# Kernel optimization log

Hardware: AMD Instinct MI355X
Metric: run time of the kernel (lower is better)

The kernel has to match this reference:

```python
import jax, jax.numpy as jnp
import numpy as np

HIDDEN = 2048
INTER = 1408
NUM_EXPERTS = 8
TOP_K = 2


def setup_inputs() -> dict:
    key = jax.random.key(0)
    k_x, k_rw, k_gu, k_dn = jax.random.split(key, 4)
    x = jax.random.normal(k_x, (2, 2048, HIDDEN), dtype=jnp.float32)
    router_weight = jax.random.normal(k_rw, (NUM_EXPERTS, HIDDEN), dtype=jnp.float32)
    gate_up_proj = jax.random.normal(k_gu, (NUM_EXPERTS, 2 * INTER, HIDDEN), dtype=jnp.float32) * 0.02
    down_proj = jax.random.normal(k_dn, (NUM_EXPERTS, HIDDEN, INTER), dtype=jnp.float32) * 0.02
    return {"x": x, "router_weight": router_weight, "gate_up_proj": gate_up_proj, "down_proj": down_proj}


def reference(x, router_weight, gate_up_proj, down_proj):
    E = router_weight.shape[0]
    xf = x.reshape(-1, x.shape[-1])  # [T, D]
    # Router: logits -> float32 softmax -> top-k -> renormalize
    logits = jnp.einsum('td,ed->te', xf, router_weight)
    scores = jax.nn.softmax(logits.astype(jnp.float32), axis=-1)
    topv, topi = jax.lax.top_k(scores, TOP_K)          # [T, K]
    topv = topv / jnp.sum(topv, axis=-1, keepdims=True)
    topv = topv.astype(logits.dtype)
    # Combine weights per (token, expert): zero for unselected experts,
    # so dense per-expert compute below reproduces the sparse dispatch math.
    comb = jnp.einsum('tk,tke->te', topv, jax.nn.one_hot(topi, E, dtype=topv.dtype))  # [T, E]
    # Per-expert SwiGLU FFN, dense over experts
    gu = jnp.einsum('td,efd->etf', xf, gate_up_proj)    # [E, T, 2*inter]
    gate, up = jnp.split(gu, 2, axis=-1)
    h = jax.nn.silu(gate) * up                          # [E, T, inter]
    eo = jnp.einsum('eti,edi->etd', h, down_proj)       # [E, T, D]
    out = jnp.einsum('etd,te->td', eo, comb)            # [T, D]
    return out
```

## Files before the change

kernel.cpp:

```cpp
#include <hip/hip_runtime.h>
#include <hip/hip_bf16.h>
#include <stdint.h>

#define HIDDEN 2048
#define INTER  1408
#define NE     8
#define NTOK   4096
#define MAXTILES 72

typedef __attribute__((ext_vector_type(8))) short short8;
typedef __attribute__((ext_vector_type(16))) float f32x16;

typedef const __attribute__((address_space(1))) unsigned char* gp1_t;
typedef __attribute__((address_space(3))) unsigned char* lp3_t;

__device__ __forceinline__ void lds_cp16(const void* g, void* l) {
    __builtin_amdgcn_global_load_lds((gp1_t)g, (lp3_t)l, 16, 0, 0);
}

__device__ __forceinline__ short8 ldswz(const __hip_bfloat16 (*S)[64], int r, int col) {
    return *(const short8*)&S[r][(((col >> 3) ^ (r & 7)) << 3)];
}

__device__ __forceinline__ float bf2f(short s) {
    union { float f; unsigned u; } u; u.u = ((unsigned)(unsigned short)s) << 16; return u.f;
}

#define C1 (NE * 2 * INTER * HIDDEN / 4)
#define C2 (NE * HIDDEN * INTER / 4)
__global__ void cvt_w_kernel(const float* __restrict__ gu, const float* __restrict__ dn,
                             __hip_bfloat16* __restrict__ gub, __hip_bfloat16* __restrict__ dnb) {
    long c = (long)blockIdx.x * blockDim.x + threadIdx.x;
    const float* s; __hip_bfloat16* d; long o;
    if (c < C1) { s = gu; d = gub; o = c; }
    else        { s = dn; d = dnb; o = c - C1; }
    o *= 4;
    float4 v = *(const float4*)(s + o);
    *(__hip_bfloat162*)(d + o)     = __float22bfloat162_rn(make_float2(v.x, v.y));
    *(__hip_bfloat162*)(d + o + 2) = __float22bfloat162_rn(make_float2(v.z, v.w));
}

__global__ void router_kernel(const float* __restrict__ x, const float* __restrict__ rw,
                              int* __restrict__ counts, int* __restrict__ topk_e,
                              float* __restrict__ topk_w, __hip_bfloat16* __restrict__ xb) {
    int wave = threadIdx.x >> 6;
    int lane = threadIdx.x & 63;
    int t = blockIdx.x * 4 + wave;
    const float4* xr = (const float4*)(x + (size_t)t * HIDDEN);
    __hip_bfloat16* xbr = xb + (size_t)t * HIDDEN;
    float acc[NE] = {0.f,0.f,0.f,0.f,0.f,0.f,0.f,0.f};
    #pragma unroll
    for (int c = lane; c < HIDDEN / 4; c += 64) {
        float4 v = xr[c];
        *(__hip_bfloat162*)(xbr + c * 4)     = __float22bfloat162_rn(make_float2(v.x, v.y));
        *(__hip_bfloat162*)(xbr + c * 4 + 2) = __float22bfloat162_rn(make_float2(v.z, v.w));
        #pragma unroll
        for (int e = 0; e < NE; ++e) {
            float4 w = ((const float4*)(rw + e * HIDDEN))[c];
            acc[e] += v.x * w.x + v.y * w.y + v.z * w.z + v.w * w.w;
        }
    }
    #pragma unroll
    for (int e = 0; e < NE; ++e) {
        #pragma unroll
        for (int off = 32; off > 0; off >>= 1) acc[e] += __shfl_xor(acc[e], off, 64);
    }
    if (lane == 0) {
        int i1 = 0; float v1 = acc[0];
        for (int e = 1; e < NE; ++e) if (acc[e] > v1) { v1 = acc[e]; i1 = e; }
        int i2 = -1; float v2 = -3.0e38f;
        for (int e = 0; e < NE; ++e) if (e != i1 && acc[e] > v2) { v2 = acc[e]; i2 = e; }
        float w1 = 1.f / (1.f + expf(v2 - v1));
        float w2 = 1.f - w1;
        topk_e[t * 2 + 0] = i1; topk_e[t * 2 + 1] = i2;
        topk_w[t * 2 + 0] = w1; topk_w[t * 2 + 1] = w2;
        atomicAdd(&counts[i1], 1);
        atomicAdd(&counts[i2], 1);
    }
}

__global__ void scan_kernel(const int* __restrict__ counts, int* __restrict__ offsets,
                            int* __restrict__ cursor, int* __restrict__ tiles,
                            int* __restrict__ n_tiles) {
    if (threadIdx.x == 0) {
        int s = 0, nt = 0;
        for (int e = 0; e < NE; ++e) {
            offsets[e] = s; cursor[e] = s;
            int c = counts[e]; s += c;
            for (int mt = 0; mt * 128 < c; ++mt) tiles[nt++] = (e << 16) | mt;
        }
        n_tiles[0] = nt;
    }
}

__global__ void scatter_kernel(const int* __restrict__ topk_e, const float* __restrict__ topk_w,
                               int* __restrict__ cursor, int* __restrict__ slot_tid,
                               float* __restrict__ slot_w, int* __restrict__ tok2slot) {
    int k = blockIdx.x * blockDim.x + threadIdx.x;
    if (k >= NTOK * 2) return;
    int e = topk_e[k];
    int slot = atomicAdd(&cursor[e], 1);
    slot_tid[slot] = k >> 1;
    slot_w[slot]   = topk_w[k];
    tok2slot[k]    = slot;
}

__global__ __launch_bounds__(256) void gemm1_kernel(
    const __hip_bfloat16* __restrict__ xb,
    const __hip_bfloat16* __restrict__ gub,
    const int* __restrict__ counts, const int* __restrict__ offsets,
    const int* __restrict__ tiles, const int* __restrict__ n_tiles,
    const int* __restrict__ slot_tid, const float* __restrict__ slot_w,
    __hip_bfloat16* __restrict__ h)
{
    const int ti = blockIdx.y;
    if (ti >= n_tiles[0]) return;
    const int tile = tiles[ti];
    const int e  = tile >> 16;
    const int mt = tile & 0xffff;
    const int nt = blockIdx.x;
    const int count = counts[e];
    const int off = offsets[e];

    __shared__ __hip_bfloat16 As[128][64];
    __shared__ __hip_bfloat16 Bs[128][64];

    const int tid  = threadIdx.x;
    const int wave = tid >> 6;
    const int lane = tid & 63;
    const int wm = wave >> 1, wn = wave & 1;
    const int l31 = lane & 31;
    const int fk  = (lane >> 5) * 8;

    const __hip_bfloat16* asrc[4];
    const __hip_bfloat16* bsrc[4];
    #pragma unroll
    for (int j = 0; j < 4; ++j) {
        int fs  = j * 256 + tid;
        int row = fs >> 3;
        int c8  = (fs & 7) ^ (row & 7);
        int rg  = mt * 128 + row;
        int rc  = rg < count ? rg : count - 1;
        int tok = slot_tid[off + rc];
        asrc[j] = xb + (size_t)tok * HIDDEN + c8 * 8;
        int within = row & 63, sel = within >> 5, idx = within & 31;
        int hc  = nt * 64 + (row >> 6) * 32 + idx;
        int grow = sel ? (INTER + hc) : hc;
        bsrc[j] = gub + ((size_t)e * 2 * INTER + grow) * HIDDEN + c8 * 8;
    }

    f32x16 accg[2], accu[2];
    #pragma unroll
    for (int mi = 0; mi < 2; ++mi) { accg[mi] = (f32x16)0.f; accu[mi] = (f32x16)0.f; }

    for (int k0 = 0; k0 < HIDDEN; k0 += 64) {
        #pragma unroll
        for (int j = 0; j < 4; ++j) {
            lds_cp16(asrc[j] + k0, (__hip_bfloat16*)As + (j * 256 + tid) * 8);
            lds_cp16(bsrc[j] + k0, (__hip_bfloat16*)Bs + (j * 256 + tid) * 8);
        }
        __syncthreads();
        #pragma unroll
        for (int kk = 0; kk < 64; kk += 16) {
            short8 a0 = ldswz(As, wm * 64 +      l31, kk + fk);
            short8 a1 = ldswz(As, wm * 64 + 32 + l31, kk + fk);
            short8 bg = ldswz(Bs, wn * 64 +      l31, kk + fk);
            short8 bu = ldswz(Bs, wn * 64 + 32 + l31, kk + fk);
            accg[0] = __builtin_amdgcn_mfma_f32_32x32x16_bf16(a0, bg, accg[0], 0, 0, 0);
            accg[1] = __builtin_amdgcn_mfma_f32_32x32x16_bf16(a1, bg, accg[1], 0, 0, 0);
            accu[0] = __builtin_amdgcn_mfma_f32_32x32x16_bf16(a0, bu, accu[0], 0, 0, 0);
            accu[1] = __builtin_amdgcn_mfma_f32_32x32x16_bf16(a1, bu, accu[1], 0, 0, 0);
        }
        __syncthreads();
    }

    #pragma unroll
    for (int mi = 0; mi < 2; ++mi) {
        #pragma unroll
        for (int reg = 0; reg < 16; ++reg) {
            int row = wm * 64 + mi * 32 + (reg & 3) + 8 * (reg >> 2) + 4 * (lane >> 5);
            int rg  = mt * 128 + row;
            if (rg < count) {
                float wgt = slot_w[off + rg];
                float g = accg[mi][reg];
                float u = accu[mi][reg];
                float hv = g / (1.f + __expf(-g)) * u * wgt;
                h[(size_t)(off + rg) * INTER + nt * 64 + wn * 32 + l31] = __float2bfloat16(hv);
            }
        }
    }
}

__global__ __launch_bounds__(256) void gemm2_kernel(
    const __hip_bfloat16* __restrict__ h,
    const __hip_bfloat16* __restrict__ dnb,
    const int* __restrict__ counts, const int* __restrict__ offsets,
    const int* __restrict__ tiles, const int* __restrict__ n_tiles,
    __hip_bfloat16* __restrict__ eo)
{
    const int ti = blockIdx.y;
    if (ti >= n_tiles[0]) return;
    const int tile = tiles[ti];
    const int e  = tile >> 16;
    const int mt = tile & 0xffff;
    const int nt = blockIdx.x;
    const int count = counts[e];
    const int off = offsets[e];

    __shared__ __hip_bfloat16 As[128][64];
    __shared__ __hip_bfloat16 Bs[128][64];

    const int tid  = threadIdx.x;
    const int wave = tid >> 6;
    const int lane = tid & 63;
    const int wm = wave >> 1, wn = wave & 1;
    const int l31 = lane & 31;
    const int fk  = (lane >> 5) * 8;

    const __hip_bfloat16* asrc[4];
    const __hip_bfloat16* bsrc[4];
    #pragma unroll
    for (int j = 0; j < 4; ++j) {
        int fs  = j * 256 + tid;
        int row = fs >> 3;
        int c8  = (fs & 7) ^ (row & 7);
        asrc[j] = h + (size_t)(off + mt * 128 + row) * INTER + c8 * 8;
        bsrc[j] = dnb + ((size_t)e * HIDDEN + nt * 128 + row) * INTER + c8 * 8;
    }

    f32x16 acc[2][2];
    #pragma unroll
    for (int mi = 0; mi < 2; ++mi)
        #pragma unroll
        for (int nj = 0; nj < 2; ++nj) acc[mi][nj] = (f32x16)0.f;

    for (int k0 = 0; k0 < INTER; k0 += 64) {
        #pragma unroll
        for (int j = 0; j < 4; ++j) {
            lds_cp16(asrc[j] + k0, (__hip_bfloat16*)As + (j * 256 + tid) * 8);
            lds_cp16(bsrc[j] + k0, (__hip_bfloat16*)Bs + (j * 256 + tid) * 8);
        }
        __syncthreads();
        #pragma unroll
        for (int kk = 0; kk < 64; kk += 16) {
            short8 a0 = ldswz(As, wm * 64 +      l31, kk + fk);
            short8 a1 = ldswz(As, wm * 64 + 32 + l31, kk + fk);
            short8 b0 = ldswz(Bs, wn * 64 +      l31, kk + fk);
            short8 b1 = ldswz(Bs, wn * 64 + 32 + l31, kk + fk);
            acc[0][0] = __builtin_amdgcn_mfma_f32_32x32x16_bf16(a0, b0, acc[0][0], 0, 0, 0);
            acc[0][1] = __builtin_amdgcn_mfma_f32_32x32x16_bf16(a0, b1, acc[0][1], 0, 0, 0);
            acc[1][0] = __builtin_amdgcn_mfma_f32_32x32x16_bf16(a1, b0, acc[1][0], 0, 0, 0);
            acc[1][1] = __builtin_amdgcn_mfma_f32_32x32x16_bf16(a1, b1, acc[1][1], 0, 0, 0);
        }
        __syncthreads();
    }

    #pragma unroll
    for (int mi = 0; mi < 2; ++mi) {
        #pragma unroll
        for (int reg = 0; reg < 16; ++reg) {
            int row = wm * 64 + mi * 32 + (reg & 3) + 8 * (reg >> 2) + 4 * (lane >> 5);
            int rg  = mt * 128 + row;
            if (rg < count) {
                size_t base = (size_t)(off + rg) * HIDDEN + nt * 128 + wn * 64;
                eo[base +      l31] = __float2bfloat16(acc[mi][0][reg]);
                eo[base + 32 + l31] = __float2bfloat16(acc[mi][1][reg]);
            }
        }
    }
}

__global__ void combine_kernel(const __hip_bfloat16* __restrict__ eo,
                               const int* __restrict__ tok2slot,
                               float* __restrict__ out) {
    int idx = blockIdx.x * blockDim.x + threadIdx.x;
    int t = idx >> 8;
    int c = (idx & 255) * 8;
    int s1 = tok2slot[t * 2], s2 = tok2slot[t * 2 + 1];
    short8 v1 = *(const short8*)(eo + (size_t)s1 * HIDDEN + c);
    short8 v2 = *(const short8*)(eo + (size_t)s2 * HIDDEN + c);
    float4 o0, o1;
    o0.x = bf2f(v1[0]) + bf2f(v2[0]); o0.y = bf2f(v1[1]) + bf2f(v2[1]);
    o0.z = bf2f(v1[2]) + bf2f(v2[2]); o0.w = bf2f(v1[3]) + bf2f(v2[3]);
    o1.x = bf2f(v1[4]) + bf2f(v2[4]); o1.y = bf2f(v1[5]) + bf2f(v2[5]);
    o1.z = bf2f(v1[6]) + bf2f(v2[6]); o1.w = bf2f(v1[7]) + bf2f(v2[7]);
    float* op = out + (size_t)t * HIDDEN + c;
    *(float4*)op = o0;
    *(float4*)(op + 4) = o1;
}

extern "C" void kernel_launch(void* const* d_in, const int* in_sizes, int n_in,
                              void* d_out, int out_size, void* d_ws, size_t ws_size,
                              hipStream_t stream)
{
    (void)in_sizes; (void)n_in; (void)ws_size; (void)out_size;
    const float* x  = (const float*)d_in[0];
    const float* rw = (const float*)d_in[1];
    const float* gu = (const float*)d_in[2];
    const float* dn = (const float*)d_in[3];

    char* p = (char*)d_ws;
    auto take = [&](size_t bytes) { char* r = p; p += (bytes + 255) & ~(size_t)255; return r; };
    __hip_bfloat16* xb  = (__hip_bfloat16*)take((size_t)NTOK * HIDDEN * 2);
    __hip_bfloat16* gub = (__hip_bfloat16*)take((size_t)NE * 2 * INTER * HIDDEN * 2);
    __hip_bfloat16* dnb = (__hip_bfloat16*)take((size_t)NE * HIDDEN * INTER * 2);
    __hip_bfloat16* hbuf= (__hip_bfloat16*)take((size_t)(2 * NTOK + 128) * INTER * 2);
    int*   counts   = (int*)take(64);
    int*   offsets  = (int*)take(64);
    int*   cursor   = (int*)take(64);
    int*   ntile    = (int*)take(64);
    int*   tiles    = (int*)take(MAXTILES * 4);
    int*   topk_e   = (int*)take((size_t)NTOK * 2 * 4);
    float* topk_w   = (float*)take((size_t)NTOK * 2 * 4);
    int*   slot_tid = (int*)take((size_t)(2 * NTOK + 128) * 4);
    float* slot_w   = (float*)take((size_t)(2 * NTOK + 128) * 4);
    int*   tok2slot = (int*)take((size_t)NTOK * 2 * 4);
    __hip_bfloat16* eo = gub;

    hipMemsetAsync(counts, 0, 64, stream);

    cvt_w_kernel<<<dim3((C1 + C2) / 256), 256, 0, stream>>>(gu, dn, gub, dnb);

    router_kernel<<<dim3(NTOK / 4), 256, 0, stream>>>(x, rw, counts, topk_e, topk_w, xb);
    scan_kernel<<<dim3(1), 64, 0, stream>>>(counts, offsets, cursor, tiles, ntile);
    scatter_kernel<<<dim3((NTOK * 2) / 256), 256, 0, stream>>>(topk_e, topk_w, cursor,
                                                               slot_tid, slot_w, tok2slot);

    gemm1_kernel<<<dim3(INTER / 64, MAXTILES), 256, 0, stream>>>(
        xb, gub, counts, offsets, tiles, ntile, slot_tid, slot_w, hbuf);
    gemm2_kernel<<<dim3(HIDDEN / 128, MAXTILES), 256, 0, stream>>>(
        hbuf, dnb, counts, offsets, tiles, ntile, eo);
    combine_kernel<<<dim3(NTOK * HIDDEN / 8 / 256), 256, 0, stream>>>(
        eo, tok2slot, (float*)d_out);
}
```

Before: 692.0 us.

## Enlarge MoE GEMM tiles with 512-thread blocks and double-buffered LDS pipeline

Both grouped GEMMs now run 512-thread blocks with larger tiles: 256x128 for gate/up and 128x256 for down. Each uses two dynamic-LDS buffers, so the next K-slice is fetched with global_load_lds while MFMAs run on the current one, and waits go through explicit vmcnt and raw barriers. The MFMA shape changes from 32x32x16 to 16x16x32, with setprio raised around the MFMA bursts, and a separate tile list is built for the larger gemm1 row tile. The aim is more reuse per loaded byte and hiding global latency behind compute. The cost is much larger LDS use, which limits occupancy, and more padding waste on partial expert tiles.

```diff
diff --git a/kernel.cpp b/kernel.cpp
--- a/kernel.cpp
+++ b/kernel.cpp
@@ -6,10 +6,11 @@
 #define INTER  1408
 #define NE     8
 #define NTOK   4096
-#define MAXTILES 72
+#define MAXT1  40
+#define MAXT2  72
 
 typedef __attribute__((ext_vector_type(8))) short short8;
-typedef __attribute__((ext_vector_type(16))) float f32x16;
+typedef __attribute__((ext_vector_type(4))) float f32x4;
 
 typedef const __attribute__((address_space(1))) unsigned char* gp1_t;
 typedef __attribute__((address_space(3))) unsigned char* lp3_t;
@@ -18,8 +19,8 @@
     __builtin_amdgcn_global_load_lds((gp1_t)g, (lp3_t)l, 16, 0, 0);
 }
 
-__device__ __forceinline__ short8 ldswz(const __hip_bfloat16 (*S)[64], int r, int col) {
-    return *(const short8*)&S[r][(((col >> 3) ^ (r & 7)) << 3)];
+__device__ __forceinline__ short8 ldswz64(const __hip_bfloat16* S, int r, int ck) {
+    return *(const short8*)&S[r * 64 + ((ck ^ (r & 7)) << 3)];
 }
 
 __device__ __forceinline__ float bf2f(short s) {
@@ -80,16 +81,18 @@
 }
 
 __global__ void scan_kernel(const int* __restrict__ counts, int* __restrict__ offsets,
-                            int* __restrict__ cursor, int* __restrict__ tiles,
-                            int* __restrict__ n_tiles) {
+                            int* __restrict__ cursor, int* __restrict__ tiles1,
+                            int* __restrict__ tiles2, int* __restrict__ n_tiles) {
     if (threadIdx.x == 0) {
-        int s = 0, nt = 0;
+        int s = 0, nt1 = 0, nt2 = 0;
         for (int e = 0; e < NE; ++e) {
             offsets[e] = s; cursor[e] = s;
             int c = counts[e]; s += c;
-            for (int mt = 0; mt * 128 < c; ++mt) tiles[nt++] = (e << 16) | mt;
-        }
-        n_tiles[0] = nt;
+            for (int mt = 0; mt * 256 < c; ++mt) tiles1[nt1++] = (e << 16) | mt;
+            for (int mt = 0; mt * 128 < c; ++mt) tiles2[nt2++] = (e << 16) | mt;
+        }
+        n_tiles[0] = nt1;
+        n_tiles[1] = nt2;
     }
 }
 
@@ -105,7 +108,7 @@
     tok2slot[k]    = slot;
 }
 
-__global__ __launch_bounds__(256) void gemm1_kernel(
+__global__ __launch_bounds__(512, 2) void gemm1_kernel(
     const __hip_bfloat16* __restrict__ xb,
     const __hip_bfloat16* __restrict__ gub,
     const int* __restrict__ counts, const int* __restrict__ offsets,
@@ -122,76 +125,111 @@
     const int count = counts[e];
     const int off = offsets[e];
 
-    __shared__ __hip_bfloat16 As[128][64];
-    __shared__ __hip_bfloat16 Bs[128][64];
+    extern __shared__ __hip_bfloat16 smem[];
+    __hip_bfloat16* A0 = smem;
+    __hip_bfloat16* B0 = smem + 16384;
+    __hip_bfloat16* A1 = smem + 32768;
+    __hip_bfloat16* B1 = smem + 49152;
 
     const int tid  = threadIdx.x;
     const int wave = tid >> 6;
     const int lane = tid & 63;
-    const int wm = wave >> 1, wn = wave & 1;
-    const int l31 = lane & 31;
-    const int fk  = (lane >> 5) * 8;
+    const int wm = wave >> 2, wn = wave & 3;
+    const int l15 = lane & 15;
+    const int q   = lane >> 4;
 
     const __hip_bfloat16* asrc[4];
     const __hip_bfloat16* bsrc[4];
     #pragma unroll
     for (int j = 0; j < 4; ++j) {
-        int fs  = j * 256 + tid;
+        int fs  = j * 512 + tid;
         int row = fs >> 3;
         int c8  = (fs & 7) ^ (row & 7);
-        int rg  = mt * 128 + row;
+        int rg  = mt * 256 + row;
         int rc  = rg < count ? rg : count - 1;
         int tok = slot_tid[off + rc];
         asrc[j] = xb + (size_t)tok * HIDDEN + c8 * 8;
-        int within = row & 63, sel = within >> 5, idx = within & 31;
-        int hc  = nt * 64 + (row >> 6) * 32 + idx;
+        int p = row >> 5, sel = (row >> 4) & 1, idx = row & 15;
+        int hc = nt * 128 + p * 16 + idx;
         int grow = sel ? (INTER + hc) : hc;
-        bsrc[j] = gub + ((size_t)e * 2 * INTER + grow) * HIDDEN + c8 * 8;
-    }
-
-    f32x16 accg[2], accu[2];
-    #pragma unroll
-    for (int mi = 0; mi < 2; ++mi) { accg[mi] = (f32x16)0.f; accu[mi] = (f32x16)0.f; }
-
-    for (int k0 = 0; k0 < HIDDEN; k0 += 64) {
-        #pragma unroll
-        for (int j = 0; j < 4; ++j) {
-            lds_cp16(asrc[j] + k0, (__hip_bfloat16*)As + (j * 256 + tid) * 8);
-            lds_cp16(bsrc[j] + k0, (__hip_bfloat16*)Bs + (j * 256 + tid) * 8);
-        }
-        __syncthreads();
-        #pragma unroll
-        for (int kk = 0; kk < 64; kk += 16) {
-            short8 a0 = ldswz(As, wm * 64 +      l31, kk + fk);
-            short8 a1 = ldswz(As, wm * 64 + 32 + l31, kk + fk);
-            short8 bg = ldswz(Bs, wn * 64 +      l31, kk + fk);
-            short8 bu = ldswz(Bs, wn * 64 + 32 + l31, kk + fk);
-            accg[0] = __builtin_amdgcn_mfma_f32_32x32x16_bf16(a0, bg, accg[0], 0, 0, 0);
-            accg[1] = __builtin_amdgcn_mfma_f32_32x32x16_bf16(a1, bg, accg[1], 0, 0, 0);
-            accu[0] = __builtin_amdgcn_mfma_f32_32x32x16_bf16(a0, bu, accu[0], 0, 0, 0);
-            accu[1] = __builtin_amdgcn_mfma_f32_32x32x16_bf16(a1, bu, accu[1], 0, 0, 0);
-        }
-        __syncthreads();
-    }
-
-    #pragma unroll
-    for (int mi = 0; mi < 2; ++mi) {
-        #pragma unroll
-        for (int reg = 0; reg < 16; ++reg) {
-            int row = wm * 64 + mi * 32 + (reg & 3) + 8 * (reg >> 2) + 4 * (lane >> 5);
-            int rg  = mt * 128 + row;
+        bsrc[j] = gub + ((size_t)(e * 2 * INTER + grow)) * HIDDEN + c8 * 8;
+    }
+
+    f32x4 acc[8][4];
+    #pragma unroll
+    for (int mf = 0; mf < 8; ++mf)
+        #pragma unroll
+        for (int nf = 0; nf < 4; ++nf) acc[mf][nf] = (f32x4)0.f;
+
+    #pragma unroll
+    for (int j = 0; j < 4; ++j) lds_cp16(asrc[j], (__hip_bfloat16*)A0 + (j * 512 + tid) * 8);
+    #pragma unroll
+    for (int j = 0; j < 4; ++j) lds_cp16(bsrc[j], (__hip_bfloat16*)B0 + (j * 512 + tid) * 8);
+
+    #pragma unroll 2
+    for (int t = 0; t < 32; ++t) {
+        const __hip_bfloat16* Ac = (t & 1) ? A1 : A0;
+        const __hip_bfloat16* Bc = (t & 1) ? B1 : B0;
+        __hip_bfloat16* An = (t & 1) ? A0 : A1;
+        __hip_bfloat16* Bn = (t & 1) ? B0 : B1;
+        if (t + 1 < 32) {
+            const int k0 = (t + 1) * 64;
+            #pragma unroll
+            for (int j = 0; j < 4; ++j) lds_cp16(asrc[j] + k0, An + (j * 512 + tid) * 8);
+            #pragma unroll
+            for (int j = 0; j < 4; ++j) lds_cp16(bsrc[j] + k0, Bn + (j * 512 + tid) * 8);
+            asm volatile("s_waitcnt vmcnt(8)" ::: "memory");
+        } else {
+            asm volatile("s_waitcnt vmcnt(0)" ::: "memory");
+        }
+        __builtin_amdgcn_sched_barrier(0);
+        __builtin_amdgcn_s_barrier();
+        asm volatile("" ::: "memory");
+        __builtin_amdgcn_sched_barrier(0);
+        #pragma unroll
+        for (int kh = 0; kh < 2; ++kh) {
+            const int ck = kh * 4 + q;
+            short8 bfr[4], afr[8];
+            #pragma unroll
+            for (int nf = 0; nf < 4; ++nf) bfr[nf] = ldswz64(Bc, wn * 64 + nf * 16 + l15, ck);
+            #pragma unroll
+            for (int mf = 0; mf < 8; ++mf) afr[mf] = ldswz64(Ac, wm * 128 + mf * 16 + l15, ck);
+            __builtin_amdgcn_s_setprio(1);
+            #pragma unroll
+            for (int mf = 0; mf < 8; ++mf)
+                #pragma unroll
+                for (int nf = 0; nf < 4; ++nf)
+                    acc[mf][nf] = __builtin_amdgcn_mfma_f32_16x16x32_bf16(afr[mf], bfr[nf], acc[mf][nf], 0, 0, 0);
+            __builtin_amdgcn_s_setprio(0);
+        }
+        __builtin_amdgcn_sched_barrier(0);
+        __builtin_amdgcn_s_barrier();
+        asm volatile("" ::: "memory");
+        __builtin_amdgcn_sched_barrier(0);
+    }
+
+    #pragma unroll
+    for (int mf = 0; mf < 8; ++mf) {
+        #pragma unroll
+        for (int reg = 0; reg < 4; ++reg) {
+            int row = wm * 128 + mf * 16 + q * 4 + reg;
+            int rg  = mt * 256 + row;
             if (rg < count) {
                 float wgt = slot_w[off + rg];
-                float g = accg[mi][reg];
-                float u = accu[mi][reg];
-                float hv = g / (1.f + __expf(-g)) * u * wgt;
-                h[(size_t)(off + rg) * INTER + nt * 64 + wn * 32 + l31] = __float2bfloat16(hv);
+                #pragma unroll
+                for (int g = 0; g < 2; ++g) {
+                    float gv = acc[mf][2 * g + 0][reg];
+                    float uv = acc[mf][2 * g + 1][reg];
+                    float hv = gv / (1.f + __expf(-gv)) * uv * wgt;
+                    h[(size_t)(off + rg) * INTER + nt * 128 + (wn * 2 + g) * 16 + l15] =
+                        __float2bfloat16(hv);
+                }
             }
         }
     }
 }
 
-__global__ __launch_bounds__(256) void gemm2_kernel(
+__global__ __launch_bounds__(512, 2) void gemm2_kernel(
     const __hip_bfloat16* __restrict__ h,
     const __hip_bfloat16* __restrict__ dnb,
     const int* __restrict__ counts, const int* __restrict__ offsets,
@@ -199,7 +237,7 @@
     __hip_bfloat16* __restrict__ eo)
 {
     const int ti = blockIdx.y;
-    if (ti >= n_tiles[0]) return;
+    if (ti >= n_tiles[1]) return;
     const int tile = tiles[ti];
     const int e  = tile >> 16;
     const int mt = tile & 0xffff;
@@ -207,64 +245,100 @@
     const int count = counts[e];
     const int off = offsets[e];
 
-    __shared__ __hip_bfloat16 As[128][64];
-    __shared__ __hip_bfloat16 Bs[128][64];
+    extern __shared__ __hip_bfloat16 smem[];
+    __hip_bfloat16* A0 = smem;
+    __hip_bfloat16* B0 = smem + 8192;
+    __hip_bfloat16* A1 = smem + 24576;
+    __hip_bfloat16* B1 = smem + 32768;
 
     const int tid  = threadIdx.x;
     const int wave = tid >> 6;
     const int lane = tid & 63;
-    const int wm = wave >> 1, wn = wave & 1;
-    const int l31 = lane & 31;
-    const int fk  = (lane >> 5) * 8;
-
-    const __hip_bfloat16* asrc[4];
+    const int wm = wave >> 2, wn = wave & 3;
+    const int l15 = lane & 15;
+    const int q   = lane >> 4;
+
+    const __hip_bfloat16* asrc[2];
     const __hip_bfloat16* bsrc[4];
     #pragma unroll
-    for (int j = 0; j < 4; ++j) {
-        int fs  = j * 256 + tid;
+    for (int j = 0; j < 2; ++j) {
+        int fs  = j * 512 + tid;
         int row = fs >> 3;
         int c8  = (fs & 7) ^ (row & 7);
         asrc[j] = h + (size_t)(off + mt * 128 + row) * INTER + c8 * 8;
-        bsrc[j] = dnb + ((size_t)e * HIDDEN + nt * 128 + row) * INTER + c8 * 8;
-    }
-
-    f32x16 acc[2][2];
-    #pragma unroll
-    for (int mi = 0; mi < 2; ++mi)
-        #pragma unroll
-        for (int nj = 0; nj < 2; ++nj) acc[mi][nj] = (f32x16)0.f;
-
-    for (int k0 = 0; k0 < INTER; k0 += 64) {
-        #pragma unroll
-        for (int j = 0; j < 4; ++j) {
-            lds_cp16(asrc[j] + k0, (__hip_bfloat16*)As + (j * 256 + tid) * 8);
-            lds_cp16(bsrc[j] + k0, (__hip_bfloat16*)Bs + (j * 256 + tid) * 8);
-        }
-        __syncthreads();
-        #pragma unroll
-        for (int kk = 0; kk < 64; kk += 16) {
-            short8 a0 = ldswz(As, wm * 64 +      l31, kk + fk);
-            short8 a1 = ldswz(As, wm * 64 + 32 + l31, kk + fk);
-            short8 b0 = ldswz(Bs, wn * 64 +      l31, kk + fk);
-            short8 b1 = ldswz(Bs, wn * 64 + 32 + l31, kk + fk);
-            acc[0][0] = __builtin_amdgcn_mfma_f32_32x32x16_bf16(a0, b0, acc[0][0], 0, 0, 0);
-            acc[0][1] = __builtin_amdgcn_mfma_f32_32x32x16_bf16(a0, b1, acc[0][1], 0, 0, 0);
-            acc[1][0] = __builtin_amdgcn_mfma_f32_32x32x16_bf16(a1, b0, acc[1][0], 0, 0, 0);
-            acc[1][1] = __builtin_amdgcn_mfma_f32_32x32x16_bf16(a1, b1, acc[1][1], 0, 0, 0);
-        }
-        __syncthreads();
-    }
-
-    #pragma unroll
-    for (int mi = 0; mi < 2; ++mi) {
-        #pragma unroll
-        for (int reg = 0; reg < 16; ++reg) {
-            int row = wm * 64 + mi * 32 + (reg & 3) + 8 * (reg >> 2) + 4 * (lane >> 5);
+    }
+    #pragma unroll
+    for (int j = 0; j < 4; ++j) {
+        int fs  = j * 512 + tid;
+        int row = fs >> 3;
+        int c8  = (fs & 7) ^ (row & 7);
+        bsrc[j] = dnb + ((size_t)(e * HIDDEN + nt * 256 + row)) * INTER + c8 * 8;
+    }
+
+    f32x4 acc[4][4];
+    #pragma unroll
+    for (int mf = 0; mf < 4; ++mf)
+        #pragma unroll
+        for (int nf = 0; nf < 4; ++nf) acc[mf][nf] = (f32x4)0.f;
+
+    #pragma unroll
+    for (int j = 0; j < 2; ++j) lds_cp16(asrc[j], (__hip_bfloat16*)A0 + (j * 512 + tid) * 8);
+    #pragma unroll
+    for (int j = 0; j < 4; ++j) lds_cp16(bsrc[j], (__hip_bfloat16*)B0 + (j * 512 + tid) * 8);
+
+    #pragma unroll 2
+    for (int t = 0; t < 22; ++t) {
+        const __hip_bfloat16* Ac = (t & 1) ? A1 : A0;
+        const __hip_bfloat16* Bc = (t & 1) ? B1 : B0;
+        __hip_bfloat16* An = (t & 1) ? A0 : A1;
+        __hip_bfloat16* Bn = (t & 1) ? B0 : B1;
+        if (t + 1 < 22) {
+            const int k0 = (t + 1) * 64;
+            #pragma unroll
+            for (int j = 0; j < 2; ++j) lds_cp16(asrc[j] + k0, An + (j * 512 + tid) * 8);
+            #pragma unroll
+            for (int j = 0; j < 4; ++j) lds_cp16(bsrc[j] + k0, Bn + (j * 512 + tid) * 8);
+            asm volatile("s_waitcnt vmcnt(6)" ::: "memory");
+        } else {
+            asm volatile("s_waitcnt vmcnt(0)" ::: "memory");
+        }
+        __builtin_amdgcn_sched_barrier(0);
+        __builtin_amdgcn_s_barrier();
+        asm volatile("" ::: "memory");
+        __builtin_amdgcn_sched_barrier(0);
+        #pragma unroll
+        for (int kh = 0; kh < 2; ++kh) {
+            const int ck = kh * 4 + q;
+            short8 bfr[4], afr[4];
+            #pragma unroll
+            for (int nf = 0; nf < 4; ++nf) bfr[nf] = ldswz64(Bc, wn * 64 + nf * 16 + l15, ck);
+            #pragma unroll
+            for (int mf = 0; mf < 4; ++mf) afr[mf] = ldswz64(Ac, wm * 64 + mf * 16 + l15, ck);
+            __builtin_amdgcn_s_setprio(1);
+            #pragma unroll
+            for (int mf = 0; mf < 4; ++mf)
+                #pragma unroll
+                for (int nf = 0; nf < 4; ++nf)
+                    acc[mf][nf] = __builtin_amdgcn_mfma_f32_16x16x32_bf16(afr[mf], bfr[nf], acc[mf][nf], 0, 0, 0);
+            __builtin_amdgcn_s_setprio(0);
+        }
+        __builtin_amdgcn_sched_barrier(0);
+        __builtin_amdgcn_s_barrier();
+        asm volatile("" ::: "memory");
+        __builtin_amdgcn_sched_barrier(0);
+    }
+
+    #pragma unroll
+    for (int mf = 0; mf < 4; ++mf) {
+        #pragma unroll
+        for (int reg = 0; reg < 4; ++reg) {
+            int row = wm * 64 + mf * 16 + q * 4 + reg;
             int rg  = mt * 128 + row;
             if (rg < count) {
-                size_t base = (size_t)(off + rg) * HIDDEN + nt * 128 + wn * 64;
-                eo[base +      l31] = __float2bfloat16(acc[mi][0][reg]);
-                eo[base + 32 + l31] = __float2bfloat16(acc[mi][1][reg]);
+                size_t base = (size_t)(off + rg) * HIDDEN + nt * 256 + wn * 64;
+                #pragma unroll
+                for (int nf = 0; nf < 4; ++nf)
+                    eo[base + nf * 16 + l15] = __float2bfloat16(acc[mf][nf][reg]);
             }
         }
     }
@@ -304,32 +378,38 @@
     __hip_bfloat16* xb  = (__hip_bfloat16*)take((size_t)NTOK * HIDDEN * 2);
     __hip_bfloat16* gub = (__hip_bfloat16*)take((size_t)NE * 2 * INTER * HIDDEN * 2);
     __hip_bfloat16* dnb = (__hip_bfloat16*)take((size_t)NE * HIDDEN * INTER * 2);
-    __hip_bfloat16* hbuf= (__hip_bfloat16*)take((size_t)(2 * NTOK + 128) * INTER * 2);
+    __hip_bfloat16* hbuf= (__hip_bfloat16*)take((size_t)(2 * NTOK + 256) * INTER * 2);
     int*   counts   = (int*)take(64);
     int*   offsets  = (int*)take(64);
     int*   cursor   = (int*)take(64);
     int*   ntile    = (int*)take(64);
-    int*   tiles    = (int*)take(MAXTILES * 4);
+    int*   tiles1   = (int*)take(MAXT1 * 4);
+    int*   tiles2   = (int*)take(MAXT2 * 4);
     int*   topk_e   = (int*)take((size_t)NTOK * 2 * 4);
     float* topk_w   = (float*)take((size_t)NTOK * 2 * 4);
-    int*   slot_tid = (int*)take((size_t)(2 * NTOK + 128) * 4);
-    float* slot_w   = (float*)take((size_t)(2 * NTOK + 128) * 4);
+    int*   slot_tid = (int*)take((size_t)(2 * NTOK + 256) * 4);
+    float* slot_w   = (float*)take((size_t)(2 * NTOK + 256) * 4);
     int*   tok2slot = (int*)take((size_t)NTOK * 2 * 4);
     __hip_bfloat16* eo = gub;
 
+    hipFuncSetAttribute((const void*)gemm1_kernel,
+                        hipFuncAttributeMaxDynamicSharedMemorySize, 131072);
+    hipFuncSetAttribute((const void*)gemm2_kernel,
+                        hipFuncAttributeMaxDynamicSharedMemorySize, 98304);
+
     hipMemsetAsync(counts, 0, 64, stream);
 
     cvt_w_kernel<<<dim3((C1 + C2) / 256), 256, 0, stream>>>(gu, dn, gub, dnb);
 
     router_kernel<<<dim3(NTOK / 4), 256, 0, stream>>>(x, rw, counts, topk_e, topk_w, xb);
-    scan_kernel<<<dim3(1), 64, 0, stream>>>(counts, offsets, cursor, tiles, ntile);
+    scan_kernel<<<dim3(1), 64, 0, stream>>>(counts, offsets, cursor, tiles1, tiles2, ntile);
     scatter_kernel<<<dim3((NTOK * 2) / 256), 256, 0, stream>>>(topk_e, topk_w, cursor,
                                                                slot_tid, slot_w, tok2slot);
 
-    gemm1_kernel<<<dim3(INTER / 64, MAXTILES), 256, 0, stream>>>(
-        xb, gub, counts, offsets, tiles, ntile, slot_tid, slot_w, hbuf);
-    gemm2_kernel<<<dim3(HIDDEN / 128, MAXTILES), 256, 0, stream>>>(
-        hbuf, dnb, counts, offsets, tiles, ntile, eo);
+    gemm1_kernel<<<dim3(INTER / 128, MAXT1), 512, 131072, stream>>>(
+        xb, gub, counts, offsets, tiles1, ntile, slot_tid, slot_w, hbuf);
+    gemm2_kernel<<<dim3(HIDDEN / 256, MAXT2), 512, 98304, stream>>>(
+        hbuf, dnb, counts, offsets, tiles2, ntile, eo);
     combine_kernel<<<dim3(NTOK * HIDDEN / 8 / 256), 256, 0, stream>>>(
         eo, tok2slot, (float*)d_out);
 }
```

Measured after the change: 738.2 us. 6.7% more time.

## Rewrite grouped MoE GEMMs as 256x256 pipelined 8-wave kernel with double-buffered LDS

Applied to the files above, without the earlier changes.

Replaces the two 128x128 single-buffered grouped GEMM kernels with one templated 512-thread kernel that computes 256x256 tiles. It uses 16x16x32 MFMAs, a swizzled 128KB dynamic LDS layout, and an explicit software pipeline in which async global-to-LDS loads for later k-tiles overlap the MFMAs, with manual vmcnt waits and barriers. The intent is more data reuse per tile and hidden load latency. In exchange it uses larger tiles, so per-expert padding waste grows, the grid has fewer blocks, and register pressure is high.

```diff
diff --git a/kernel.cpp b/kernel.cpp
--- a/kernel.cpp
+++ b/kernel.cpp
@@ -6,20 +6,16 @@
 #define INTER  1408
 #define NE     8
 #define NTOK   4096
-#define MAXTILES 72
+#define MAXT   40
 
 typedef __attribute__((ext_vector_type(8))) short short8;
-typedef __attribute__((ext_vector_type(16))) float f32x16;
+typedef __attribute__((ext_vector_type(4))) float f32x4;
 
 typedef const __attribute__((address_space(1))) unsigned char* gp1_t;
 typedef __attribute__((address_space(3))) unsigned char* lp3_t;
 
 __device__ __forceinline__ void lds_cp16(const void* g, void* l) {
     __builtin_amdgcn_global_load_lds((gp1_t)g, (lp3_t)l, 16, 0, 0);
-}
-
-__device__ __forceinline__ short8 ldswz(const __hip_bfloat16 (*S)[64], int r, int col) {
-    return *(const short8*)&S[r][(((col >> 3) ^ (r & 7)) << 3)];
 }
 
 __device__ __forceinline__ float bf2f(short s) {
@@ -87,7 +83,7 @@
         for (int e = 0; e < NE; ++e) {
             offsets[e] = s; cursor[e] = s;
             int c = counts[e]; s += c;
-            for (int mt = 0; mt * 128 < c; ++mt) tiles[nt++] = (e << 16) | mt;
+            for (int mt = 0; mt * 256 < c; ++mt) tiles[nt++] = (e << 16) | mt;
         }
         n_tiles[0] = nt;
     }
@@ -105,14 +101,71 @@
     tok2slot[k]    = slot;
 }
 
-__global__ __launch_bounds__(256) void gemm1_kernel(
-    const __hip_bfloat16* __restrict__ xb,
-    const __hip_bfloat16* __restrict__ gub,
+
+#define FENCE asm volatile("" ::: "memory")
+#define W_V8  asm volatile("s_waitcnt vmcnt(8)" ::: "memory")
+#define W_V4  asm volatile("s_waitcnt vmcnt(4)" ::: "memory")
+#define W_V0  asm volatile("s_waitcnt vmcnt(0)" ::: "memory")
+#define W_NONE do {} while (0)
+#define BAR do { __builtin_amdgcn_sched_barrier(0); FENCE; \
+                 __builtin_amdgcn_s_barrier(); FENCE; } while (0)
+#define LGKM0 do { asm volatile("s_waitcnt lgkmcnt(0)" ::: "memory"); \
+                   __builtin_amdgcn_sched_barrier(0); } while (0)
+
+#define DSA(Rg, mf) (*(const short8*)((Rg) + laneA + (mf) * 512))
+#define DSB(Rg, nf) (*(const short8*)((Rg) + laneB + (nf) * 512))
+
+#define MFMA16(NFP) do { \
+    __builtin_amdgcn_s_setprio(1); \
+    _Pragma("unroll") \
+    for (int mf_ = 0; mf_ < 8; ++mf_) { \
+        acc[mf_][(NFP)*2+0] = __builtin_amdgcn_mfma_f32_16x16x32_bf16(afr[mf_], bfr[0], acc[mf_][(NFP)*2+0], 0, 0, 0); \
+        acc[mf_][(NFP)*2+1] = __builtin_amdgcn_mfma_f32_16x16x32_bf16(afr[mf_], bfr[1], acc[mf_][(NFP)*2+1], 0, 0, 0); \
+    } \
+    __builtin_amdgcn_s_setprio(0); \
+    __builtin_amdgcn_sched_barrier(0); \
+} while (0)
+
+#define KTILE(T, S01, S23, W1, W3) do { \
+    const int b_ = (T) & 1; \
+    const __hip_bfloat16* RA0_ = smem + (((b_ << 2) | 0) << 13); \
+    const __hip_bfloat16* RA1_ = smem + (((b_ << 2) | 1) << 13); \
+    const __hip_bfloat16* RB0_ = smem + (((b_ << 2) | 2) << 13); \
+    const __hip_bfloat16* RB1_ = smem + (((b_ << 2) | 3) << 13); \
+     \
+    _Pragma("unroll") for (int mf_ = 0; mf_ < 8; ++mf_) afr[mf_] = DSA(RA0_, mf_); \
+    bfr[0] = DSB(RB0_, 0); bfr[1] = DSB(RB0_, 1); \
+    if (S01) stage(0, 1, (T) + 1, b_ ^ 1); \
+    LGKM0; MFMA16(0); BAR; \
+     \
+    bfr[0] = DSB(RB0_, 2); bfr[1] = DSB(RB0_, 3); \
+    if (S01) stage(1, 1, (T) + 1, b_ ^ 1); \
+    LGKM0; MFMA16(1); \
+    W1; BAR; \
+     \
+    _Pragma("unroll") for (int mf_ = 0; mf_ < 8; ++mf_) afr[mf_] = DSA(RA1_, mf_); \
+    bfr[0] = DSB(RB1_, 0); bfr[1] = DSB(RB1_, 1); \
+    if (S23) stage(0, 0, (T) + 2, b_); \
+    LGKM0; MFMA16(0); BAR; \
+     \
+    bfr[0] = DSB(RB1_, 2); bfr[1] = DSB(RB1_, 3); \
+    if (S23) stage(1, 0, (T) + 2, b_); \
+    LGKM0; MFMA16(1); \
+    W3; BAR; \
+} while (0)
+
+template<int WHICH>
+__global__ __launch_bounds__(512, 2) void moe_gemm(
+    const __hip_bfloat16* __restrict__ Ag,
+    const __hip_bfloat16* __restrict__ Bg,
     const int* __restrict__ counts, const int* __restrict__ offsets,
     const int* __restrict__ tiles, const int* __restrict__ n_tiles,
     const int* __restrict__ slot_tid, const float* __restrict__ slot_w,
-    __hip_bfloat16* __restrict__ h)
+    __hip_bfloat16* __restrict__ Out)
 {
+    constexpr int KDIM = (WHICH == 1) ? HIDDEN : INTER;
+    constexpr int NT   = KDIM / 64;
+
     const int ti = blockIdx.y;
     if (ti >= n_tiles[0]) return;
     const int tile = tiles[ti];
@@ -122,149 +175,103 @@
     const int count = counts[e];
     const int off = offsets[e];
 
-    __shared__ __hip_bfloat16 As[128][64];
-    __shared__ __hip_bfloat16 Bs[128][64];
+    extern __shared__ __hip_bfloat16 smem[];
 
     const int tid  = threadIdx.x;
     const int wave = tid >> 6;
     const int lane = tid & 63;
-    const int wm = wave >> 1, wn = wave & 1;
-    const int l31 = lane & 31;
-    const int fk  = (lane >> 5) * 8;
-
-    const __hip_bfloat16* asrc[4];
-    const __hip_bfloat16* bsrc[4];
+    const int wm = wave >> 2, wn = wave & 3;
+    const int l15 = lane & 15;
+    const int q   = lane >> 4;
+    const int sw  = (l15 >> 1) & 3;
+
+    const int laneA = (wm * 128 + l15) * 32 + ((q ^ sw) << 3);
+    const int laneB = (wn * 64  + l15) * 32 + ((q ^ sw) << 3);
+
+    const __hip_bfloat16* PA[2];
+    const __hip_bfloat16* PB[2];
     #pragma unroll
-    for (int j = 0; j < 4; ++j) {
-        int fs  = j * 256 + tid;
-        int row = fs >> 3;
-        int c8  = (fs & 7) ^ (row & 7);
-        int rg  = mt * 128 + row;
+    for (int j = 0; j < 2; ++j) {
+        int cs  = j * 512 + tid;
+        int row = cs >> 2;
+        int kc  = (cs & 3) ^ ((row >> 1) & 3);
+        int rg  = mt * 256 + row;
         int rc  = rg < count ? rg : count - 1;
-        int tok = slot_tid[off + rc];
-        asrc[j] = xb + (size_t)tok * HIDDEN + c8 * 8;
-        int within = row & 63, sel = within >> 5, idx = within & 31;
-        int hc  = nt * 64 + (row >> 6) * 32 + idx;
-        int grow = sel ? (INTER + hc) : hc;
-        bsrc[j] = gub + ((size_t)e * 2 * INTER + grow) * HIDDEN + c8 * 8;
-    }
-
-    f32x16 accg[2], accu[2];
+        if constexpr (WHICH == 1) {
+            int tok = slot_tid[off + rc];
+            PA[j] = Ag + (size_t)tok * HIDDEN + kc * 8;
+            int p = row >> 5, sel = (row >> 4) & 1, idx = row & 15;
+            int hc = nt * 128 + p * 16 + idx;
+            int grow = sel ? (INTER + hc) : hc;
+            PB[j] = Bg + ((size_t)(e * 2 * INTER + grow)) * HIDDEN + kc * 8;
+        } else {
+            PA[j] = Ag + (size_t)(off + rc) * INTER + kc * 8;
+            PB[j] = Bg + ((size_t)(e * HIDDEN + nt * 256 + row)) * INTER + kc * 8;
+        }
+    }
+
+    auto stage = [&](int m, int kh, int kt, int b) {
+        __hip_bfloat16* L = smem + (size_t)(((b << 2) | (m << 1) | kh) << 13);
+        const __hip_bfloat16* s0 = (m ? PB[0] : PA[0]) + kt * 64 + kh * 32;
+        const __hip_bfloat16* s1 = (m ? PB[1] : PA[1]) + kt * 64 + kh * 32;
+        lds_cp16(s0, L + tid * 8);
+        lds_cp16(s1, L + (512 + tid) * 8);
+    };
+
+    f32x4 acc[8][4];
     #pragma unroll
-    for (int mi = 0; mi < 2; ++mi) { accg[mi] = (f32x16)0.f; accu[mi] = (f32x16)0.f; }
-
-    for (int k0 = 0; k0 < HIDDEN; k0 += 64) {
-        #pragma unroll
-        for (int j = 0; j < 4; ++j) {
-            lds_cp16(asrc[j] + k0, (__hip_bfloat16*)As + (j * 256 + tid) * 8);
-            lds_cp16(bsrc[j] + k0, (__hip_bfloat16*)Bs + (j * 256 + tid) * 8);
-        }
-        __syncthreads();
-        #pragma unroll
-        for (int kk = 0; kk < 64; kk += 16) {
-            short8 a0 = ldswz(As, wm * 64 +      l31, kk + fk);
-            short8 a1 = ldswz(As, wm * 64 + 32 + l31, kk + fk);
-            short8 bg = ldswz(Bs, wn * 64 +      l31, kk + fk);
-            short8 bu = ldswz(Bs, wn * 64 + 32 + l31, kk + fk);
-            accg[0] = __builtin_amdgcn_mfma_f32_32x32x16_bf16(a0, bg, accg[0], 0, 0, 0);
-            accg[1] = __builtin_amdgcn_mfma_f32_32x32x16_bf16(a1, bg, accg[1], 0, 0, 0);
-            accu[0] = __builtin_amdgcn_mfma_f32_32x32x16_bf16(a0, bu, accu[0], 0, 0, 0);
-            accu[1] = __builtin_amdgcn_mfma_f32_32x32x16_bf16(a1, bu, accu[1], 0, 0, 0);
-        }
-        __syncthreads();
-    }
-
-    #pragma unroll
-    for (int mi = 0; mi < 2; ++mi) {
-        #pragma unroll
-        for (int reg = 0; reg < 16; ++reg) {
-            int row = wm * 64 + mi * 32 + (reg & 3) + 8 * (reg >> 2) + 4 * (lane >> 5);
-            int rg  = mt * 128 + row;
-            if (rg < count) {
-                float wgt = slot_w[off + rg];
-                float g = accg[mi][reg];
-                float u = accu[mi][reg];
-                float hv = g / (1.f + __expf(-g)) * u * wgt;
-                h[(size_t)(off + rg) * INTER + nt * 64 + wn * 32 + l31] = __float2bfloat16(hv);
+    for (int mf = 0; mf < 8; ++mf)
+        #pragma unroll
+        for (int nf = 0; nf < 4; ++nf) acc[mf][nf] = (f32x4)0.f;
+
+    short8 afr[8], bfr[2];
+
+    stage(0, 0, 0, 0); stage(1, 0, 0, 0);
+    stage(0, 1, 0, 0); stage(1, 1, 0, 0);
+    stage(0, 0, 1, 1); stage(1, 0, 1, 1);
+    W_V8; BAR;
+
+    #pragma unroll 2
+    for (int t = 0; t < NT - 2; ++t) {
+        KTILE(t, 1, 1, W_V8, W_V8);
+    }
+    KTILE(NT - 2, 1, 0, W_V8, W_V4);
+    KTILE(NT - 1, 0, 0, W_V0, W_NONE);
+    W_V0;
+
+    if constexpr (WHICH == 1) {
+        #pragma unroll
+        for (int mf = 0; mf < 8; ++mf) {
+            #pragma unroll
+            for (int reg = 0; reg < 4; ++reg) {
+                int row = wm * 128 + mf * 16 + q * 4 + reg;
+                int rg  = mt * 256 + row;
+                if (rg < count) {
+                    float wgt = slot_w[off + rg];
+                    #pragma unroll
+                    for (int g = 0; g < 2; ++g) {
+                        float gv = acc[mf][2 * g + 0][reg];
+                        float uv = acc[mf][2 * g + 1][reg];
+                        float hv = gv / (1.f + __expf(-gv)) * uv * wgt;
+                        Out[(size_t)(off + rg) * INTER + nt * 128 + (wn * 2 + g) * 16 + l15] =
+                            __float2bfloat16(hv);
+                    }
+                }
             }
         }
-    }
-}
-
-__global__ __launch_bounds__(256) void gemm2_kernel(
-    const __hip_bfloat16* __restrict__ h,
-    const __hip_bfloat16* __restrict__ dnb,
-    const int* __restrict__ counts, const int* __restrict__ offsets,
-    const int* __restrict__ tiles, const int* __restrict__ n_tiles,
-    __hip_bfloat16* __restrict__ eo)
-{
-    const int ti = blockIdx.y;
-    if (ti >= n_tiles[0]) return;
-    const int tile = tiles[ti];
-    const int e  = tile >> 16;
-    const int mt = tile & 0xffff;
-    const int nt = blockIdx.x;
-    const int count = counts[e];
-    const int off = offsets[e];
-
-    __shared__ __hip_bfloat16 As[128][64];
-    __shared__ __hip_bfloat16 Bs[128][64];
-
-    const int tid  = threadIdx.x;
-    const int wave = tid >> 6;
-    const int lane = tid & 63;
-    const int wm = wave >> 1, wn = wave & 1;
-    const int l31 = lane & 31;
-    const int fk  = (lane >> 5) * 8;
-
-    const __hip_bfloat16* asrc[4];
-    const __hip_bfloat16* bsrc[4];
-    #pragma unroll
-    for (int j = 0; j < 4; ++j) {
-        int fs  = j * 256 + tid;
-        int row = fs >> 3;
-        int c8  = (fs & 7) ^ (row & 7);
-        asrc[j] = h + (size_t)(off + mt * 128 + row) * INTER + c8 * 8;
-        bsrc[j] = dnb + ((size_t)e * HIDDEN + nt * 128 + row) * INTER + c8 * 8;
-    }
-
-    f32x16 acc[2][2];
-    #pragma unroll
-    for (int mi = 0; mi < 2; ++mi)
-        #pragma unroll
-        for (int nj = 0; nj < 2; ++nj) acc[mi][nj] = (f32x16)0.f;
-
-    for (int k0 = 0; k0 < INTER; k0 += 64) {
-        #pragma unroll
-        for (int j = 0; j < 4; ++j) {
-            lds_cp16(asrc[j] + k0, (__hip_bfloat16*)As + (j * 256 + tid) * 8);
-            lds_cp16(bsrc[j] + k0, (__hip_bfloat16*)Bs + (j * 256 + tid) * 8);
-        }
-        __syncthreads();
-        #pragma unroll
-        for (int kk = 0; kk < 64; kk += 16) {
-            short8 a0 = ldswz(As, wm * 64 +      l31, kk + fk);
-            short8 a1 = ldswz(As, wm * 64 + 32 + l31, kk + fk);
-            short8 b0 = ldswz(Bs, wn * 64 +      l31, kk + fk);
-            short8 b1 = ldswz(Bs, wn * 64 + 32 + l31, kk + fk);
-            acc[0][0] = __builtin_amdgcn_mfma_f32_32x32x16_bf16(a0, b0, acc[0][0], 0, 0, 0);
-            acc[0][1] = __builtin_amdgcn_mfma_f32_32x32x16_bf16(a0, b1, acc[0][1], 0, 0, 0);
-            acc[1][0] = __builtin_amdgcn_mfma_f32_32x32x16_bf16(a1, b0, acc[1][0], 0, 0, 0);
-            acc[1][1] = __builtin_amdgcn_mfma_f32_32x32x16_bf16(a1, b1, acc[1][1], 0, 0, 0);
-        }
-        __syncthreads();
-    }
-
-    #pragma unroll
-    for (int mi = 0; mi < 2; ++mi) {
-        #pragma unroll
-        for (int reg = 0; reg < 16; ++reg) {
-            int row = wm * 64 + mi * 32 + (reg & 3) + 8 * (reg >> 2) + 4 * (lane >> 5);
-            int rg  = mt * 128 + row;
-            if (rg < count) {
-                size_t base = (size_t)(off + rg) * HIDDEN + nt * 128 + wn * 64;
-                eo[base +      l31] = __float2bfloat16(acc[mi][0][reg]);
-                eo[base + 32 + l31] = __float2bfloat16(acc[mi][1][reg]);
+    } else {
+        #pragma unroll
+        for (int mf = 0; mf < 8; ++mf) {
+            #pragma unroll
+            for (int reg = 0; reg < 4; ++reg) {
+                int row = wm * 128 + mf * 16 + q * 4 + reg;
+                int rg  = mt * 256 + row;
+                if (rg < count) {
+                    size_t base = (size_t)(off + rg) * HIDDEN + nt * 256 + wn * 64;
+                    #pragma unroll
+                    for (int nf = 0; nf < 4; ++nf)
+                        Out[base + nf * 16 + l15] = __float2bfloat16(acc[mf][nf][reg]);
+                }
             }
         }
     }
@@ -304,18 +311,23 @@
     __hip_bfloat16* xb  = (__hip_bfloat16*)take((size_t)NTOK * HIDDEN * 2);
     __hip_bfloat16* gub = (__hip_bfloat16*)take((size_t)NE * 2 * INTER * HIDDEN * 2);
     __hip_bfloat16* dnb = (__hip_bfloat16*)take((size_t)NE * HIDDEN * INTER * 2);
-    __hip_bfloat16* hbuf= (__hip_bfloat16*)take((size_t)(2 * NTOK + 128) * INTER * 2);
+    __hip_bfloat16* hbuf= (__hip_bfloat16*)take((size_t)(2 * NTOK + 256) * INTER * 2);
     int*   counts   = (int*)take(64);
     int*   offsets  = (int*)take(64);
     int*   cursor   = (int*)take(64);
     int*   ntile    = (int*)take(64);
-    int*   tiles    = (int*)take(MAXTILES * 4);
+    int*   tiles    = (int*)take(MAXT * 4);
     int*   topk_e   = (int*)take((size_t)NTOK * 2 * 4);
     float* topk_w   = (float*)take((size_t)NTOK * 2 * 4);
-    int*   slot_tid = (int*)take((size_t)(2 * NTOK + 128) * 4);
-    float* slot_w   = (float*)take((size_t)(2 * NTOK + 128) * 4);
+    int*   slot_tid = (int*)take((size_t)(2 * NTOK + 256) * 4);
+    float* slot_w   = (float*)take((size_t)(2 * NTOK + 256) * 4);
     int*   tok2slot = (int*)take((size_t)NTOK * 2 * 4);
     __hip_bfloat16* eo = gub;
+
+    hipFuncSetAttribute((const void*)moe_gemm<1>,
+                        hipFuncAttributeMaxDynamicSharedMemorySize, 131072);
+    hipFuncSetAttribute((const void*)moe_gemm<2>,
+                        hipFuncAttributeMaxDynamicSharedMemorySize, 131072);
 
     hipMemsetAsync(counts, 0, 64, stream);
 
@@ -326,10 +338,10 @@
     scatter_kernel<<<dim3((NTOK * 2) / 256), 256, 0, stream>>>(topk_e, topk_w, cursor,
                                                                slot_tid, slot_w, tok2slot);
 
-    gemm1_kernel<<<dim3(INTER / 64, MAXTILES), 256, 0, stream>>>(
+    moe_gemm<1><<<dim3(INTER / 128, MAXT), 512, 131072, stream>>>(
         xb, gub, counts, offsets, tiles, ntile, slot_tid, slot_w, hbuf);
-    gemm2_kernel<<<dim3(HIDDEN / 128, MAXTILES), 256, 0, stream>>>(
-        hbuf, dnb, counts, offsets, tiles, ntile, eo);
+    moe_gemm<2><<<dim3(HIDDEN / 256, MAXT), 512, 131072, stream>>>(
+        hbuf, dnb, counts, offsets, tiles, ntile, slot_tid, slot_w, eo);
     combine_kernel<<<dim3(NTOK * HIDDEN / 8 / 256), 256, 0, stream>>>(
         eo, tok2slot, (float*)d_out);
 }
```

After: 667.8 us. -3.5%, faster.
